# Kernel tuning notes

Hardware: AMD Instinct MI355X
Metric: run time of the kernel (lower is better)

The kernel has to match this reference:

```python
import jax, jax.numpy as jnp
import numpy as np

N, D_IN, D_OUT, B = 200000, 256, 256, 256

def setup_inputs() -> dict:
    key = jax.random.key(0)
    k1, k2, k3, k4, k5 = jax.random.split(key, 5)
    lim = float(np.sqrt(6.0 / (D_IN + D_OUT)))  # xavier_init scale=1
    return {
        "nodes": jax.random.normal(k1, (N, D_IN), dtype=jnp.float32),
        "owner_masks": jax.random.randint(k2, (B, N), 0, 2, dtype=jnp.int32),
        "Wt": jax.random.uniform(k3, (D_OUT, D_IN), jnp.float32, -lim, lim),
        "bt": jax.random.normal(k4, (D_OUT,), dtype=jnp.float32),
        "Wg": jax.random.uniform(k5, (D_OUT, D_IN), jnp.float32, -lim, lim),
        "bg": jnp.ones((D_OUT,), dtype=jnp.float32),  # gate bias init fill_(1)
    }

def reference(nodes, owner_masks, Wt, bt, Wg, bg):
    # gates = sigmoid(Linear(nodes)); data = Linear(nodes)  -> [N, D_OUT]
    gates = jax.nn.sigmoid(nodes @ Wg.T + bg)
    data = nodes @ Wt.T + bt
    # owner-mask matmul == masked scatter-sum over nodes -> [B, D_OUT]
    fmask = owner_masks.astype(jnp.float32)
    res = jnp.einsum('bn,nd->bd', fmask, data * gates)
    return res  # dropout is identity in eval mode
```

## Files before the change

kernel.cpp:

```cpp
#include <hip/hip_runtime.h>
#include <stdint.h>

#define NND 200000

typedef unsigned short u16;
typedef __attribute__((ext_vector_type(4))) float f4;
typedef __attribute__((ext_vector_type(4))) int   i4;
typedef __attribute__((ext_vector_type(2))) unsigned int u2;
typedef __attribute__((ext_vector_type(8))) short s8;
typedef __attribute__((ext_vector_type(4))) float acc4;

__device__ __forceinline__ short f2bf(float f) {
    union { float f; uint32_t u; } v; v.f = f;
    uint32_t r = v.u + 0x7FFFu + ((v.u >> 16) & 1u);
    return (short)(r >> 16);
}
__device__ __forceinline__ uint32_t pack2bf(float a, float b) {
    uint32_t ua = __float_as_uint(a), ub = __float_as_uint(b);
    ua = ua + 0x7FFFu + ((ua >> 16) & 1u);
    ub = ub + 0x7FFFu + ((ub >> 16) & 1u);
    return (ua >> 16) | (ub & 0xFFFF0000u);
}
__device__ __forceinline__ void gld16(const void* g, void* l) {
    __builtin_amdgcn_global_load_lds(
        (const __attribute__((address_space(1))) void*)g,
        (__attribute__((address_space(3))) void*)l, 16, 0, 0);
}

__global__ __launch_bounds__(256) void k_prep(const float* __restrict__ Wt,
                                              const float* __restrict__ Wg,
                                              u16* __restrict__ wtb,
                                              u16* __restrict__ wgb) {
    int i = blockIdx.x * 256 + threadIdx.x;
    wtb[i] = (u16)f2bf(Wt[i]);
    wgb[i] = (u16)f2bf(Wg[i]);
}

__global__ __launch_bounds__(1024, 4) void k_h(const float* __restrict__ nodes,
                                               const u16* __restrict__ wtb,
                                               const u16* __restrict__ wgb,
                                               const float* __restrict__ btp,
                                               const float* __restrict__ bgp,
                                               u16* __restrict__ h_t) {
    __shared__ __align__(16) char smem[69632];
    char* A0 = smem;
    char* A1 = smem + 16384;
    char* H0 = smem + 32768;
    char* H1 = smem + 51200;

    const int tid  = threadIdx.x;
    const int lane = tid & 63, wave = tid >> 6;
    const int quad = lane >> 4, l16 = lane & 15;
    const int dgl  = wave * 16 + l16;

    s8 wT[8], wG[8];
    {
        const u16* wtp = wtb + dgl * 256 + quad * 8;
        const u16* wgp = wgb + dgl * 256 + quad * 8;
#pragma unroll
        for (int ks = 0; ks < 8; ++ks) {
            wT[ks] = *(const s8*)(wtp + ks * 32);
            wG[ks] = *(const s8*)(wgp + ks * 32);
        }
    }
    const float btv = btp[dgl], bgv = bgp[dgl];

    const int c0   = blockIdx.x * 25;
    const int arow = tid >> 5, akq = tid & 31;
    const int awbyte = akq * 512 + (((arow & 24) | ((arow ^ akq) & 7)) << 4);
    const int sd = tid >> 2, sc = tid & 3;

    f4 ar0, ar1;
    {
        const f4* p = (const f4*)(nodes + (size_t)(c0 * 32 + arow) * 256 + akq * 8);
        ar0 = p[0]; ar1 = p[1];
        i4 aw;
        aw.x = (int)pack2bf(ar0.x, ar0.y); aw.y = (int)pack2bf(ar0.z, ar0.w);
        aw.z = (int)pack2bf(ar1.x, ar1.y); aw.w = (int)pack2bf(ar1.z, ar1.w);
        *(i4*)(A0 + awbyte) = aw;
        const f4* q = (const f4*)(nodes + (size_t)((c0 + 1) * 32 + arow) * 256 + akq * 8);
        ar0 = q[0]; ar1 = q[1];
    }
    __syncthreads();

    char *Ard = A0, *Awr = A1, *Hwr = H0, *Hrd = H1;

    for (int c = 0; c < 25; ++c) {
        acc4 at0 = (acc4)0.0f, at1 = (acc4)0.0f, ag0 = (acc4)0.0f, ag1 = (acc4)0.0f;
#pragma unroll
        for (int ks = 0; ks < 8; ++ks) {
            const int kq = ks * 4 + quad;
            const int ab = kq * 512 + (((l16 & 8) | ((l16 ^ kq) & 7)) << 4);
            s8 af0 = *(const s8*)(Ard + ab);
            s8 af1 = *(const s8*)(Ard + ab + 256);
            at0 = __builtin_amdgcn_mfma_f32_16x16x32_bf16(af0, wT[ks], at0, 0, 0, 0);
            ag0 = __builtin_amdgcn_mfma_f32_16x16x32_bf16(af0, wG[ks], ag0, 0, 0, 0);
            at1 = __builtin_amdgcn_mfma_f32_16x16x32_bf16(af1, wT[ks], at1, 0, 0, 0);
            ag1 = __builtin_amdgcn_mfma_f32_16x16x32_bf16(af1, wG[ks], ag1, 0, 0, 0);
        }
        if (c < 24) {
            i4 aw;
            aw.x = (int)pack2bf(ar0.x, ar0.y); aw.y = (int)pack2bf(ar0.z, ar0.w);
            aw.z = (int)pack2bf(ar1.x, ar1.y); aw.w = (int)pack2bf(ar1.z, ar1.w);
            *(i4*)(Awr + awbyte) = aw;
        }
        if (c < 23) {
            const f4* p = (const f4*)(nodes + (size_t)((c0 + c + 2) * 32 + arow) * 256 + akq * 8);
            ar0 = p[0]; ar1 = p[1];
        }
#pragma unroll
        for (int rt = 0; rt < 2; ++rt) {
            const acc4 t = rt ? at1 : at0;
            const acc4 g = rt ? ag1 : ag0;
            float h0 = (t[0] + btv) / (1.0f + __expf(-(g[0] + bgv)));
            float h1 = (t[1] + btv) / (1.0f + __expf(-(g[1] + bgv)));
            float h2 = (t[2] + btv) / (1.0f + __expf(-(g[2] + bgv)));
            float h3 = (t[3] + btv) / (1.0f + __expf(-(g[3] + bgv)));
            u2 p; p.x = pack2bf(h0, h1); p.y = pack2bf(h2, h3);
            *(u2*)(Hwr + dgl * 72 + rt * 32 + quad * 8) = p;
        }
        if (c > 0) {
            f4 v = *(const f4*)(Hrd + sd * 72 + sc * 16);
            *(f4*)(h_t + (size_t)sd * NND + (size_t)(c0 + c - 1) * 32 + sc * 8) = v;
        }
        __syncthreads();
        char* tp = Ard; Ard = Awr; Awr = tp;
        tp = Hwr; Hwr = Hrd; Hrd = tp;
    }
    {
        f4 v = *(const f4*)(Hrd + sd * 72 + sc * 16);
        *(f4*)(h_t + (size_t)sd * NND + (size_t)(c0 + 24) * 32 + sc * 8) = v;
    }
}

__global__ __launch_bounds__(512, 4) void k_res(const int* __restrict__ masks,
                                                const u16* __restrict__ h_t,
                                                float* __restrict__ outp) {
    __shared__ __align__(16) char smem[49152];
    u16* Ms = (u16*)smem;
    u16* Hs = (u16*)(smem + 16384);

    const int tid  = threadIdx.x;
    const int lane = tid & 63, wave = tid >> 6;
    const int quad = lane >> 4, l16 = lane & 15;
    const int bh = wave & 1, dq = wave >> 1;
    const int b0 = blockIdx.x * 128;
    const int nbase = blockIdx.y * 960;
    const int R = min(15, (NND - nbase) / 64);

    acc4 acc[4][4];
#pragma unroll
    for (int rt = 0; rt < 4; ++rt)
#pragma unroll
        for (int dt = 0; dt < 4; ++dt) acc[rt][dt] = (acc4)0.0f;

    const int mr0 = tid >> 3, mc0 = tid & 7;
    const int mr1 = (512 + tid) >> 3, mc1 = tid & 7;
    i4 mp[2][2];
    {
        const i4* p0 = (const i4*)(masks + (size_t)(b0 + mr0) * NND + nbase + mc0 * 8);
        const i4* p1 = (const i4*)(masks + (size_t)(b0 + mr1) * NND + nbase + mc1 * 8);
        mp[0][0] = p0[0]; mp[0][1] = p0[1];
        mp[1][0] = p1[0]; mp[1][1] = p1[1];
    }

    for (int it = 0; it < R; ++it) {
        const int nb = nbase + it * 64;
#pragma unroll
        for (int i = 0; i < 4; ++i) {
            int g = i * 512 + tid;
            int dr = g >> 3, c = g & 7;
            gld16(h_t + (size_t)dr * NND + nb + ((c ^ (dr & 7)) << 3), (char*)Hs + g * 16);
        }
#pragma unroll
        for (int i = 0; i < 2; ++i) {
            int mr = (i == 0) ? mr0 : mr1, c = (i == 0) ? mc0 : mc1;
            i4 w;
            w.x = (int)((((uint32_t)(-mp[i][0].x)) & 0x3F80u) | ((((uint32_t)(-mp[i][0].y)) & 0x3F80u) << 16));
            w.y = (int)((((uint32_t)(-mp[i][0].z)) & 0x3F80u) | ((((uint32_t)(-mp[i][0].w)) & 0x3F80u) << 16));
            w.z = (int)((((uint32_t)(-mp[i][1].x)) & 0x3F80u) | ((((uint32_t)(-mp[i][1].y)) & 0x3F80u) << 16));
            w.w = (int)((((uint32_t)(-mp[i][1].z)) & 0x3F80u) | ((((uint32_t)(-mp[i][1].w)) & 0x3F80u) << 16));
            *(i4*)((char*)Ms + mr * 128 + ((c ^ (mr & 7)) << 4)) = w;
        }
        __syncthreads();
        if (it + 1 < R) {
            const int nn = nb + 64;
            const i4* p0 = (const i4*)(masks + (size_t)(b0 + mr0) * NND + nn + mc0 * 8);
            const i4* p1 = (const i4*)(masks + (size_t)(b0 + mr1) * NND + nn + mc1 * 8);
            mp[0][0] = p0[0]; mp[0][1] = p0[1];
            mp[1][0] = p1[0]; mp[1][1] = p1[1];
        }
#pragma unroll
        for (int ks = 0; ks < 2; ++ks) {
            const int q = (ks << 2) | quad;
            s8 af[4];
#pragma unroll
            for (int rt = 0; rt < 4; ++rt) {
                int r = bh * 64 + rt * 16 + l16;
                af[rt] = *(const s8*)((char*)Ms + r * 128 + ((q ^ (l16 & 7)) << 4));
            }
#pragma unroll
            for (int dt = 0; dt < 4; ++dt) {
                int dl = dq * 64 + dt * 16 + l16;
                s8 bf_ = *(const s8*)((char*)Hs + dl * 128 + ((q ^ (dl & 7)) << 4));
#pragma unroll
                for (int rt = 0; rt < 4; ++rt)
                    acc[rt][dt] = __builtin_amdgcn_mfma_f32_16x16x32_bf16(af[rt], bf_, acc[rt][dt], 0, 0, 0);
            }
        }
        __syncthreads();
    }
#pragma unroll
    for (int rt = 0; rt < 4; ++rt)
#pragma unroll
        for (int dt = 0; dt < 4; ++dt) {
            int b = b0 + bh * 64 + rt * 16 + quad * 4;
            int d = dq * 64 + dt * 16 + l16;
#pragma unroll
            for (int r = 0; r < 4; ++r)
                atomicAdd(outp + (size_t)(b + r) * 256 + d, acc[rt][dt][r]);
        }
}

extern "C" void kernel_launch(void* const* d_in, const int* in_sizes, int n_in,
                              void* d_out, int out_size, void* d_ws, size_t ws_size,
                              hipStream_t stream) {
    const float* nodes = (const float*)d_in[0];
    const int*   masks = (const int*)d_in[1];
    const float* Wt    = (const float*)d_in[2];
    const float* bt    = (const float*)d_in[3];
    const float* Wg    = (const float*)d_in[4];
    const float* bg    = (const float*)d_in[5];
    float* outp = (float*)d_out;

    u16* h_t = (u16*)d_ws;
    u16* wtb = (u16*)((char*)d_ws + (size_t)102400000);
    u16* wgb = wtb + 65536;

    hipMemsetAsync(d_out, 0, (size_t)out_size * sizeof(float), stream);
    k_prep<<<dim3(256), dim3(256), 0, stream>>>(Wt, Wg, wtb, wgb);
    k_h<<<dim3(250), dim3(1024), 0, stream>>>(nodes, wtb, wgb, bt, bg, h_t);
    k_res<<<dim3(2, 209), dim3(512), 0, stream>>>(masks, h_t, outp);
}
```

Measured before the change: 498.0 us.

## Double-buffer k_res with async LDS loads and rebalance grids across CUs

k_h now runs 500 blocks of 12-13 chunks instead of 250 blocks of 25 chunks, spreading the nodes GEMM across more CUs. k_res is rebuilt as 256 blocks of 1024 threads, each covering all 256 batch rows over a contiguous span of node tiles. It double-buffers the mask and h tiles in 128KB of LDS, issuing the next tile's global_load_lds before the current MFMAs and waiting with partial vmcnt. It also swaps __syncthreads for a barrier that only waits on lgkmcnt. Together these aim to hide memory latency and improve load balance, at the cost of LDS occupancy (one block per CU) and hand-tuned waitcnt correctness.

```diff
diff --git a/kernel.cpp b/kernel.cpp
--- a/kernel.cpp
+++ b/kernel.cpp
@@ -25,6 +25,11 @@
     __builtin_amdgcn_global_load_lds(
         (const __attribute__((address_space(1))) void*)g,
         (__attribute__((address_space(3))) void*)l, 16, 0, 0);
+}
+__device__ __forceinline__ void bar_lgkm() {
+    asm volatile("s_waitcnt lgkmcnt(0)" ::: "memory");
+    __builtin_amdgcn_s_barrier();
+    asm volatile("" ::: "memory");
 }
 
 __global__ __launch_bounds__(256) void k_prep(const float* __restrict__ Wt,
@@ -65,7 +70,10 @@
     }
     const float btv = btp[dgl], bgv = bgp[dgl];
 
-    const int c0   = blockIdx.x * 25;
+    const int bid = blockIdx.x;
+    const int NC  = (bid < 250) ? 13 : 12;
+    const int c0  = (bid < 250) ? bid * 13 : 3250 + (bid - 250) * 12;
+
     const int arow = tid >> 5, akq = tid & 31;
     const int awbyte = akq * 512 + (((arow & 24) | ((arow ^ akq) & 7)) << 4);
     const int sd = tid >> 2, sc = tid & 3;
@@ -81,11 +89,11 @@
         const f4* q = (const f4*)(nodes + (size_t)((c0 + 1) * 32 + arow) * 256 + akq * 8);
         ar0 = q[0]; ar1 = q[1];
     }
-    __syncthreads();
+    bar_lgkm();
 
     char *Ard = A0, *Awr = A1, *Hwr = H0, *Hrd = H1;
 
-    for (int c = 0; c < 25; ++c) {
+    for (int c = 0; c < NC; ++c) {
         acc4 at0 = (acc4)0.0f, at1 = (acc4)0.0f, ag0 = (acc4)0.0f, ag1 = (acc4)0.0f;
 #pragma unroll
         for (int ks = 0; ks < 8; ++ks) {
@@ -98,13 +106,13 @@
             at1 = __builtin_amdgcn_mfma_f32_16x16x32_bf16(af1, wT[ks], at1, 0, 0, 0);
             ag1 = __builtin_amdgcn_mfma_f32_16x16x32_bf16(af1, wG[ks], ag1, 0, 0, 0);
         }
-        if (c < 24) {
+        if (c < NC - 1) {
             i4 aw;
             aw.x = (int)pack2bf(ar0.x, ar0.y); aw.y = (int)pack2bf(ar0.z, ar0.w);
             aw.z = (int)pack2bf(ar1.x, ar1.y); aw.w = (int)pack2bf(ar1.z, ar1.w);
             *(i4*)(Awr + awbyte) = aw;
         }
-        if (c < 23) {
+        if (c < NC - 2) {
             const f4* p = (const f4*)(nodes + (size_t)((c0 + c + 2) * 32 + arow) * 256 + akq * 8);
             ar0 = p[0]; ar1 = p[1];
         }
@@ -123,30 +131,31 @@
             f4 v = *(const f4*)(Hrd + sd * 72 + sc * 16);
             *(f4*)(h_t + (size_t)sd * NND + (size_t)(c0 + c - 1) * 32 + sc * 8) = v;
         }
-        __syncthreads();
+        bar_lgkm();
         char* tp = Ard; Ard = Awr; Awr = tp;
         tp = Hwr; Hwr = Hrd; Hrd = tp;
     }
     {
         f4 v = *(const f4*)(Hrd + sd * 72 + sc * 16);
-        *(f4*)(h_t + (size_t)sd * NND + (size_t)(c0 + 24) * 32 + sc * 8) = v;
-    }
-}
-
-__global__ __launch_bounds__(512, 4) void k_res(const int* __restrict__ masks,
-                                                const u16* __restrict__ h_t,
-                                                float* __restrict__ outp) {
-    __shared__ __align__(16) char smem[49152];
-    u16* Ms = (u16*)smem;
-    u16* Hs = (u16*)(smem + 16384);
+        *(f4*)(h_t + (size_t)sd * NND + (size_t)(c0 + NC - 1) * 32 + sc * 8) = v;
+    }
+}
+
+__global__ __launch_bounds__(1024, 4) void k_res(const int* __restrict__ masks,
+                                                 const u16* __restrict__ h_t,
+                                                 float* __restrict__ outp) {
+    __shared__ __align__(16) char smem[131072];
+    char* Ms0 = smem;
+    char* Hs0 = smem + 65536;
 
     const int tid  = threadIdx.x;
     const int lane = tid & 63, wave = tid >> 6;
     const int quad = lane >> 4, l16 = lane & 15;
-    const int bh = wave & 1, dq = wave >> 1;
-    const int b0 = blockIdx.x * 128;
-    const int nbase = blockIdx.y * 960;
-    const int R = min(15, (NND - nbase) / 64);
+    const int bh = wave & 3, dq = wave >> 2;
+
+    const int bid = blockIdx.x;
+    const int R   = 12 + (bid < 53 ? 1 : 0);
+    const int it0 = bid * 12 + min(bid, 53);
 
     acc4 acc[4][4];
 #pragma unroll
@@ -154,42 +163,62 @@
 #pragma unroll
         for (int dt = 0; dt < 4; ++dt) acc[rt][dt] = (acc4)0.0f;
 
-    const int mr0 = tid >> 3, mc0 = tid & 7;
-    const int mr1 = (512 + tid) >> 3, mc1 = tid & 7;
-    i4 mp[2][2];
-    {
-        const i4* p0 = (const i4*)(masks + (size_t)(b0 + mr0) * NND + nbase + mc0 * 8);
-        const i4* p1 = (const i4*)(masks + (size_t)(b0 + mr1) * NND + nbase + mc1 * 8);
-        mp[0][0] = p0[0]; mp[0][1] = p0[1];
-        mp[1][0] = p1[0]; mp[1][1] = p1[1];
-    }
-
+    const int mr = tid >> 2, seg = tid & 3;
+    const size_t mrow = (size_t)mr * NND;
+
+    i4 mp[4];
+    {
+        const int nb = it0 * 64;
+        const i4* p = (const i4*)(masks + mrow + nb + seg * 16);
+        mp[0] = p[0]; mp[1] = p[1]; mp[2] = p[2]; mp[3] = p[3];
+#pragma unroll
+        for (int i = 0; i < 2; ++i) {
+            int g = i * 1024 + tid;
+            int dr = g >> 3, c = g & 7;
+            gld16(h_t + (size_t)dr * NND + nb + ((c ^ (dr & 7)) << 3), Hs0 + g * 16);
+        }
+    }
+
+    int cur = 0;
     for (int it = 0; it < R; ++it) {
-        const int nb = nbase + it * 64;
-#pragma unroll
-        for (int i = 0; i < 4; ++i) {
-            int g = i * 512 + tid;
-            int dr = g >> 3, c = g & 7;
-            gld16(h_t + (size_t)dr * NND + nb + ((c ^ (dr & 7)) << 3), (char*)Hs + g * 16);
-        }
-#pragma unroll
-        for (int i = 0; i < 2; ++i) {
-            int mr = (i == 0) ? mr0 : mr1, c = (i == 0) ? mc0 : mc1;
-            i4 w;
-            w.x = (int)((((uint32_t)(-mp[i][0].x)) & 0x3F80u) | ((((uint32_t)(-mp[i][0].y)) & 0x3F80u) << 16));
-            w.y = (int)((((uint32_t)(-mp[i][0].z)) & 0x3F80u) | ((((uint32_t)(-mp[i][0].w)) & 0x3F80u) << 16));
-            w.z = (int)((((uint32_t)(-mp[i][1].x)) & 0x3F80u) | ((((uint32_t)(-mp[i][1].y)) & 0x3F80u) << 16));
-            w.w = (int)((((uint32_t)(-mp[i][1].z)) & 0x3F80u) | ((((uint32_t)(-mp[i][1].w)) & 0x3F80u) << 16));
-            *(i4*)((char*)Ms + mr * 128 + ((c ^ (mr & 7)) << 4)) = w;
-        }
-        __syncthreads();
+        const int nb = (it0 + it) * 64;
+        {
+            uint32_t w0 = (((uint32_t)(-mp[0].x)) & 0x3F80u) | ((((uint32_t)(-mp[0].y)) & 0x3F80u) << 16);
+            uint32_t w1 = (((uint32_t)(-mp[0].z)) & 0x3F80u) | ((((uint32_t)(-mp[0].w)) & 0x3F80u) << 16);
+            uint32_t w2 = (((uint32_t)(-mp[1].x)) & 0x3F80u) | ((((uint32_t)(-mp[1].y)) & 0x3F80u) << 16);
+            uint32_t w3 = (((uint32_t)(-mp[1].z)) & 0x3F80u) | ((((uint32_t)(-mp[1].w)) & 0x3F80u) << 16);
+            uint32_t w4 = (((uint32_t)(-mp[2].x)) & 0x3F80u) | ((((uint32_t)(-mp[2].y)) & 0x3F80u) << 16);
+            uint32_t w5 = (((uint32_t)(-mp[2].z)) & 0x3F80u) | ((((uint32_t)(-mp[2].w)) & 0x3F80u) << 16);
+            uint32_t w6 = (((uint32_t)(-mp[3].x)) & 0x3F80u) | ((((uint32_t)(-mp[3].y)) & 0x3F80u) << 16);
+            uint32_t w7 = (((uint32_t)(-mp[3].z)) & 0x3F80u) | ((((uint32_t)(-mp[3].w)) & 0x3F80u) << 16);
+            i4 a, b;
+            a.x = (int)w0; a.y = (int)w1; a.z = (int)w2; a.w = (int)w3;
+            b.x = (int)w4; b.y = (int)w5; b.z = (int)w6; b.w = (int)w7;
+            char* base = Ms0 + cur * 32768 + mr * 128;
+            const int g0 = seg * 2;
+            *(i4*)(base + (((g0    ) ^ (mr & 7)) << 4)) = a;
+            *(i4*)(base + (((g0 + 1) ^ (mr & 7)) << 4)) = b;
+        }
         if (it + 1 < R) {
-            const int nn = nb + 64;
-            const i4* p0 = (const i4*)(masks + (size_t)(b0 + mr0) * NND + nn + mc0 * 8);
-            const i4* p1 = (const i4*)(masks + (size_t)(b0 + mr1) * NND + nn + mc1 * 8);
-            mp[0][0] = p0[0]; mp[0][1] = p0[1];
-            mp[1][0] = p1[0]; mp[1][1] = p1[1];
-        }
+            const i4* p = (const i4*)(masks + mrow + (nb + 64) + seg * 16);
+            mp[0] = p[0]; mp[1] = p[1]; mp[2] = p[2]; mp[3] = p[3];
+        }
+        bar_lgkm();
+        if (it + 1 < R) {
+#pragma unroll
+            for (int i = 0; i < 2; ++i) {
+                int g = i * 1024 + tid;
+                int dr = g >> 3, c = g & 7;
+                gld16(h_t + (size_t)dr * NND + (nb + 64) + ((c ^ (dr & 7)) << 3),
+                      Hs0 + (cur ^ 1) * 32768 + g * 16);
+            }
+            asm volatile("s_waitcnt vmcnt(6)" ::: "memory");
+        } else {
+            asm volatile("s_waitcnt vmcnt(0)" ::: "memory");
+        }
+        __builtin_amdgcn_sched_barrier(0);
+        const char* Mr = Ms0 + cur * 32768;
+        const char* Hr = Hs0 + cur * 32768;
 #pragma unroll
         for (int ks = 0; ks < 2; ++ks) {
             const int q = (ks << 2) | quad;
@@ -197,24 +226,24 @@
 #pragma unroll
             for (int rt = 0; rt < 4; ++rt) {
                 int r = bh * 64 + rt * 16 + l16;
-                af[rt] = *(const s8*)((char*)Ms + r * 128 + ((q ^ (l16 & 7)) << 4));
+                af[rt] = *(const s8*)(Mr + r * 128 + ((q ^ (r & 7)) << 4));
             }
 #pragma unroll
             for (int dt = 0; dt < 4; ++dt) {
                 int dl = dq * 64 + dt * 16 + l16;
-                s8 bf_ = *(const s8*)((char*)Hs + dl * 128 + ((q ^ (dl & 7)) << 4));
+                s8 bf_ = *(const s8*)(Hr + dl * 128 + ((q ^ (dl & 7)) << 4));
 #pragma unroll
                 for (int rt = 0; rt < 4; ++rt)
                     acc[rt][dt] = __builtin_amdgcn_mfma_f32_16x16x32_bf16(af[rt], bf_, acc[rt][dt], 0, 0, 0);
             }
         }
-        __syncthreads();
+        cur ^= 1;
     }
 #pragma unroll
     for (int rt = 0; rt < 4; ++rt)
 #pragma unroll
         for (int dt = 0; dt < 4; ++dt) {
-            int b = b0 + bh * 64 + rt * 16 + quad * 4;
+            int b = bh * 64 + rt * 16 + quad * 4;
             int d = dq * 64 + dt * 16 + l16;
 #pragma unroll
             for (int r = 0; r < 4; ++r)
@@ -239,6 +268,6 @@
 
     hipMemsetAsync(d_out, 0, (size_t)out_size * sizeof(float), stream);
     k_prep<<<dim3(256), dim3(256), 0, stream>>>(Wt, Wg, wtb, wgb);
-    k_h<<<dim3(250), dim3(1024), 0, stream>>>(nodes, wtb, wgb, bt, bg, h_t);
-    k_res<<<dim3(2, 209), dim3(512), 0, stream>>>(masks, h_t, outp);
-}
+    k_h<<<dim3(500), dim3(1024), 0, stream>>>(nodes, wtb, wgb, bt, bg, h_t);
+    k_res<<<dim3(256), dim3(1024), 0, stream>>>(masks, h_t, outp);
+}
```

After: 513.4 us. 1.03x slower.
